# Kernel tuning notes

Measured on AMD Instinct MI355X. Metric: run time of the kernel, lower is better.

## Reference

```python
import jax, jax.numpy as jnp
import numpy as np
from jax import lax

ACTIVE_TOKENS = 256

def setup_inputs() -> dict:
    key = jax.random.key(0)
    k1, k2, k3, k4, k5 = jax.random.split(key, 5)
    B, L, D, A = 8, 4096, 1024, 256
    return {
        "x": jax.random.normal(k1, (B, L, D), dtype=jnp.float32),
        "active": jax.random.normal(k2, (B, A, D), dtype=jnp.float32),
        "cold": jax.random.normal(k3, (B, D), dtype=jnp.float32),
        "w_sal": jax.random.normal(k4, (D,), dtype=jnp.float32) * 0.02,
        "w_read": jax.random.normal(k5, (D, D), dtype=jnp.float32) * 0.02,
    }

def reference(x, active, cold, w_sal, w_read):
    # combined: [B, A+L, D]
    combined = jnp.concatenate([active, x], axis=1)
    B, Lc, D = combined.shape
    keep = min(ACTIVE_TOKENS, Lc)
    # salience head: Linear(D, 1, bias=False) -> [B, Lc]
    salience = jnp.einsum("bld,d->bl", combined, w_sal)
    _, top_idx = lax.top_k(salience, keep)          # [B, keep]
    top_idx = jnp.sort(top_idx, axis=-1)
    # gather kept tokens; torch detaches new_active before use
    kept = jnp.take_along_axis(combined, top_idx[:, :, None], axis=1)  # [B, keep, D]
    new_active = lax.stop_gradient(kept)
    # dropped-token mean (masked_select compaction == total minus kept)
    n_dropped = Lc - keep  # static > 0 here
    dropped_mean = (combined.sum(axis=1) - kept.sum(axis=1)) / n_dropped  # [B, D]
    cold_new = 0.9 * cold + 0.1 * dropped_mean
    # contexts and residual read projection
    active_ctx = new_active.mean(axis=1)            # [B, D]
    ctx = active_ctx + cold_new                      # [B, D]
    x_out = x + jnp.einsum("bd,ed->be", ctx, w_read)[:, None, :]  # Linear: ctx @ W^T
    return x_out, new_active, lax.stop_gradient(cold_new)
```

## Files before the change

kernel.cpp:

```cpp
#include <hip/hip_runtime.h>

#define B 8
#define XROWS 4096
#define AROWS 256
#define LC 4352
#define DD 1024
#define KEEP 256

typedef float vfloat4 __attribute__((ext_vector_type(4)));

__device__ __forceinline__ void nt_store4(const float4& v, float* p) {
    vfloat4 t = {v.x, v.y, v.z, v.w};
    __builtin_nontemporal_store(t, (vfloat4*)p);
}

__device__ __forceinline__ const float* combined_row(const float* __restrict__ x,
                                                     const float* __restrict__ act,
                                                     int b, int l) {
    return (l < AROWS) ? (act + ((size_t)b * AROWS + l) * DD)
                       : (x + ((size_t)b * XROWS + (l - AROWS)) * DD);
}

__global__ __launch_bounds__(256) void k_zero(float* __restrict__ p, int n) {
    int i = blockIdx.x * 256 + threadIdx.x;
    if (i < n) p[i] = 0.0f;
}

__global__ __launch_bounds__(256) void k_sal_sums(
        const float* __restrict__ x, const float* __restrict__ act,
        const float* __restrict__ wsal, float* __restrict__ sal,
        float* __restrict__ sums) {
    const int tid  = threadIdx.x;
    const int wave = tid >> 6;
    const int lane = tid & 63;
    const int b     = blockIdx.x / 136;
    const int chunk = blockIdx.x % 136;
    const int row0  = chunk * 32;
    const int c0 = lane * 4;

    const float4 w0 = *(const float4*)(wsal + 0 * 256 + c0);
    const float4 w1 = *(const float4*)(wsal + 1 * 256 + c0);
    const float4 w2 = *(const float4*)(wsal + 2 * 256 + c0);
    const float4 w3 = *(const float4*)(wsal + 3 * 256 + c0);

    float4 s0 = make_float4(0,0,0,0), s1 = s0, s2 = s0, s3 = s0;

    for (int r = wave; r < 32; r += 4) {
        const int l = row0 + r;
        const float* rp = combined_row(x, act, b, l);
        const float4 a0 = *(const float4*)(rp + 0 * 256 + c0);
        const float4 a1 = *(const float4*)(rp + 1 * 256 + c0);
        const float4 a2 = *(const float4*)(rp + 2 * 256 + c0);
        const float4 a3 = *(const float4*)(rp + 3 * 256 + c0);
        s0.x += a0.x; s0.y += a0.y; s0.z += a0.z; s0.w += a0.w;
        s1.x += a1.x; s1.y += a1.y; s1.z += a1.z; s1.w += a1.w;
        s2.x += a2.x; s2.y += a2.y; s2.z += a2.z; s2.w += a2.w;
        s3.x += a3.x; s3.y += a3.y; s3.z += a3.z; s3.w += a3.w;
        float s = a0.x*w0.x + a0.y*w0.y + a0.z*w0.z + a0.w*w0.w
                + a1.x*w1.x + a1.y*w1.y + a1.z*w1.z + a1.w*w1.w
                + a2.x*w2.x + a2.y*w2.y + a2.z*w2.z + a2.w*w2.w
                + a3.x*w3.x + a3.y*w3.y + a3.z*w3.z + a3.w*w3.w;
        #pragma unroll
        for (int m = 32; m >= 1; m >>= 1) s += __shfl_xor(s, m, 64);
        if (lane == 0) sal[b * LC + l] = s;
    }

    __shared__ float acc[4][DD];
    float* aw = acc[wave];
    *(float4*)(aw + 0 * 256 + c0) = s0;
    *(float4*)(aw + 1 * 256 + c0) = s1;
    *(float4*)(aw + 2 * 256 + c0) = s2;
    *(float4*)(aw + 3 * 256 + c0) = s3;
    __syncthreads();
    const int col = tid * 4;
    float4 t0 = *(const float4*)(acc[0] + col);
    float4 t1 = *(const float4*)(acc[1] + col);
    float4 t2 = *(const float4*)(acc[2] + col);
    float4 t3 = *(const float4*)(acc[3] + col);
    float* sb = sums + b * DD;
    atomicAdd(sb + col + 0, t0.x + t1.x + t2.x + t3.x);
    atomicAdd(sb + col + 1, t0.y + t1.y + t2.y + t3.y);
    atomicAdd(sb + col + 2, t0.z + t1.z + t2.z + t3.z);
    atomicAdd(sb + col + 3, t0.w + t1.w + t2.w + t3.w);
}

__global__ __launch_bounds__(1024) void k_topk(const float* __restrict__ sal,
                                               int* __restrict__ idx,
                                               float* __restrict__ ksum) {
    const int b = blockIdx.x;
    const int tid = threadIdx.x;
    const int lane = tid & 63;
    __shared__ unsigned keys[LC];
    __shared__ int hist[256];
    __shared__ int wtot4[4];
    __shared__ int wtot16[16];
    __shared__ unsigned prefS;
    __shared__ int kremS;

    if (tid < DD) ksum[b * DD + tid] = 0.0f;

    for (int i = tid; i < LC; i += 1024) {
        unsigned u = __float_as_uint(sal[b * LC + i]);
        keys[i] = (u & 0x80000000u) ? ~u : (u | 0x80000000u);
    }
    if (tid == 0) { prefS = 0u; kremS = KEEP; }
    __syncthreads();

    for (int pass = 0; pass < 4; ++pass) {
        const int shift = 24 - 8 * pass;
        if (tid < 256) hist[tid] = 0;
        __syncthreads();
        const unsigned pref = prefS;
        const int krem = kremS;
        for (int i = tid; i < LC; i += 1024) {
            const unsigned k = keys[i];
            if (pass == 0 || (k >> (shift + 8)) == (pref >> (shift + 8)))
                atomicAdd(&hist[(k >> shift) & 255], 1);
        }
        __syncthreads();
        int h = 0, cum = 0;
        if (tid < 256) {
            h = hist[tid];
            cum = h;
            #pragma unroll
            for (int off = 1; off <= 32; off <<= 1) {
                int v = __shfl_down(cum, off, 64);
                if (lane + off < 64) cum += v;
            }
            if (lane == 0) wtot4[tid >> 6] = cum;
        }
        __syncthreads();
        if (tid < 256) {
            for (int w2 = (tid >> 6) + 1; w2 < 4; ++w2) cum += wtot4[w2];
            if (cum >= krem && (cum - h) < krem) {
                prefS = pref | ((unsigned)tid << shift);
                kremS = krem - (cum - h);
            }
        }
        __syncthreads();
    }

    const unsigned T = prefS;
    const int needEQ = kremS;

    const int start = tid * 5;
    const int end = (start + 5 < LC) ? (start + 5) : LC;
    int gt = 0, eq = 0;
    for (int i = start; i < end; ++i) {
        const unsigned k = keys[i];
        gt += (k > T);
        eq += (k == T);
    }
    int packed = (gt << 16) | eq;
    int p = packed;
    #pragma unroll
    for (int off = 1; off <= 32; off <<= 1) {
        int v = __shfl_up(p, off, 64);
        if (lane >= off) p += v;
    }
    if (lane == 63) wtot16[tid >> 6] = p;
    __syncthreads();
    int base = 0;
    for (int w2 = 0; w2 < (tid >> 6); ++w2) base += wtot16[w2];
    const int exc = p - packed + base;
    int gtB = exc >> 16;
    int eqB = exc & 0xFFFF;
    for (int i = start; i < end; ++i) {
        const unsigned k = keys[i];
        if (k > T) {
            idx[b * KEEP + gtB + min(eqB, needEQ)] = i;
            ++gtB;
        } else if (k == T) {
            if (eqB < needEQ) idx[b * KEEP + gtB + eqB] = i;
            ++eqB;
        }
    }
}

__global__ __launch_bounds__(256) void k_gather(const float* __restrict__ x,
        const float* __restrict__ act, const int* __restrict__ idx,
        float* __restrict__ out_active, float* __restrict__ ksum) {
    const int b = blockIdx.x >> 3;
    const int chunk = blockIdx.x & 7;
    const int tid = threadIdx.x;
    const int c4 = tid * 4;
    float4 cs = make_float4(0,0,0,0);
    for (int r = 0; r < 32; ++r) {
        const int k = chunk * 32 + r;
        const int l = idx[b * KEEP + k];
        const float4 v = *(const float4*)(combined_row(x, act, b, l) + c4);
        nt_store4(v, out_active + ((size_t)b * KEEP + k) * DD + c4);
        cs.x += v.x; cs.y += v.y; cs.z += v.z; cs.w += v.w;
    }
    float* kb = ksum + b * DD;
    atomicAdd(kb + c4 + 0, cs.x);
    atomicAdd(kb + c4 + 1, cs.y);
    atomicAdd(kb + c4 + 2, cs.z);
    atomicAdd(kb + c4 + 3, cs.w);
}

__global__ __launch_bounds__(256) void k_read(const float* __restrict__ sums,
        const float* __restrict__ ksum, const float* __restrict__ cold,
        const float* __restrict__ wread, float* __restrict__ rvec,
        float* __restrict__ out_cold) {
    const int e = blockIdx.x;
    const int tid = threadIdx.x;
    const int wave = tid >> 6;
    const int lane = tid & 63;
    const int c4 = tid * 4;
    __shared__ float ctxs[B][DD];
    __shared__ float part[4][B];

    #pragma unroll
    for (int bb = 0; bb < B; ++bb) {
        const float4 s  = *(const float4*)(sums + bb * DD + c4);
        const float4 ks = *(const float4*)(ksum + bb * DD + c4);
        const float4 cd = *(const float4*)(cold + bb * DD + c4);
        float4 cn, cx;
        cn.x = 0.9f * cd.x + 0.1f * ((s.x - ks.x) * (1.0f / 4096.0f));
        cn.y = 0.9f * cd.y + 0.1f * ((s.y - ks.y) * (1.0f / 4096.0f));
        cn.z = 0.9f * cd.z + 0.1f * ((s.z - ks.z) * (1.0f / 4096.0f));
        cn.w = 0.9f * cd.w + 0.1f * ((s.w - ks.w) * (1.0f / 4096.0f));
        cx.x = ks.x * (1.0f / 256.0f) + cn.x;
        cx.y = ks.y * (1.0f / 256.0f) + cn.y;
        cx.z = ks.z * (1.0f / 256.0f) + cn.z;
        cx.w = ks.w * (1.0f / 256.0f) + cn.w;
        *(float4*)(&ctxs[bb][c4]) = cx;
        if (e == 0) *(float4*)(out_cold + bb * DD + c4) = cn;
    }
    __syncthreads();

    const float4 w = *(const float4*)(wread + (size_t)e * DD + c4);
    float p[B];
    #pragma unroll
    for (int bb = 0; bb < B; ++bb) {
        const float4 c = *(const float4*)(&ctxs[bb][c4]);
        p[bb] = w.x*c.x + w.y*c.y + w.z*c.z + w.w*c.w;
    }
    #pragma unroll
    for (int bb = 0; bb < B; ++bb) {
        #pragma unroll
        for (int m = 32; m >= 1; m >>= 1) p[bb] += __shfl_xor(p[bb], m, 64);
        if (lane == 0) part[wave][bb] = p[bb];
    }
    __syncthreads();
    if (tid < B) rvec[tid * DD + e] = part[0][tid] + part[1][tid] + part[2][tid] + part[3][tid];
}

__global__ __launch_bounds__(256) void k_xout(const float* __restrict__ x,
        const float* __restrict__ rvec, float* __restrict__ xout) {
    const size_t total = (size_t)B * XROWS * (DD / 4);
    const float4* x4 = (const float4*)x;
    const float4* r4 = (const float4*)rvec;
    float* of = (float*)xout;
    for (size_t i = (size_t)blockIdx.x * 256 + threadIdx.x; i < total;
         i += (size_t)gridDim.x * 256) {
        float4 v = x4[i];
        const int e4 = (int)(i & 255);
        const int bb = (int)(i >> 20);
        const float4 r = r4[(bb << 8) | e4];
        v.x += r.x; v.y += r.y; v.z += r.z; v.w += r.w;
        nt_store4(v, of + i * 4);
    }
}

extern "C" void kernel_launch(void* const* d_in, const int* in_sizes, int n_in,
                              void* d_out, int out_size, void* d_ws, size_t ws_size,
                              hipStream_t stream) {
    (void)in_sizes; (void)n_in; (void)out_size; (void)ws_size;
    const float* x     = (const float*)d_in[0];
    const float* act   = (const float*)d_in[1];
    const float* cold  = (const float*)d_in[2];
    const float* wsal  = (const float*)d_in[3];
    const float* wread = (const float*)d_in[4];

    float* out        = (float*)d_out;
    float* xout       = out;
    float* out_active = xout + (size_t)B * XROWS * DD;
    float* out_cold   = out_active + (size_t)B * KEEP * DD;

    float* ws   = (float*)d_ws;
    float* sal  = ws;
    float* sums = sal + B * LC;
    float* ksum = sums + B * DD;
    float* rvec = ksum + B * DD;
    int*   idx  = (int*)(rvec + B * DD);

    k_zero<<<(B * DD + 255) / 256, 256, 0, stream>>>(sums, B * DD);
    k_sal_sums<<<B * 136, 256, 0, stream>>>(x, act, wsal, sal, sums);
    k_topk<<<B, 1024, 0, stream>>>(sal, idx, ksum);
    k_gather<<<B * 8, 256, 0, stream>>>(x, act, idx, out_active, ksum);
    k_read<<<DD, 256, 0, stream>>>(sums, ksum, cold, wread, rvec, out_cold);
    k_xout<<<8192, 256, 0, stream>>>(x, rvec, xout);
}
```

Baseline: 305.8 us.

## Fuse all stages into one cooperative persistent kernel with grid syncs

Replaces the six separate launches (zero, salience/sums, top-k, gather, read projection, x_out) with a single cooperative kernel of 256 blocks of 1024 threads, separated by grid.sync barriers. Block-level partial sums are reduced in shared memory before atomics, and zeroing of the accumulators moves into the first phase. The aim is to remove launch gaps and inter-kernel tails. The cost is fewer resident blocks in the bandwidth-heavy phases, only 8 of 256 blocks doing work during top-k, and the overhead of grid-wide barriers.

```diff
diff --git a/kernel.cpp b/kernel.cpp
--- a/kernel.cpp
+++ b/kernel.cpp
@@ -1,4 +1,7 @@
 #include <hip/hip_runtime.h>
+#include <hip/hip_cooperative_groups.h>
+
+namespace cg = cooperative_groups;
 
 #define B 8
 #define XROWS 4096
@@ -6,6 +9,9 @@
 #define LC 4352
 #define DD 1024
 #define KEEP 256
+#define NBLK 256
+#define NTHR 1024
+#define P1ROWS 136
 
 typedef float vfloat4 __attribute__((ext_vector_type(4)));
 
@@ -21,246 +27,263 @@
                        : (x + ((size_t)b * XROWS + (l - AROWS)) * DD);
 }
 
-__global__ __launch_bounds__(256) void k_zero(float* __restrict__ p, int n) {
-    int i = blockIdx.x * 256 + threadIdx.x;
-    if (i < n) p[i] = 0.0f;
-}
-
-__global__ __launch_bounds__(256) void k_sal_sums(
+__global__ __launch_bounds__(NTHR, 4) void k_fused(
         const float* __restrict__ x, const float* __restrict__ act,
-        const float* __restrict__ wsal, float* __restrict__ sal,
-        float* __restrict__ sums) {
+        const float* __restrict__ cold, const float* __restrict__ wsal,
+        const float* __restrict__ wread,
+        float* __restrict__ xout, float* __restrict__ out_active,
+        float* __restrict__ out_cold,
+        float* __restrict__ sal, float* __restrict__ sums,
+        float* __restrict__ ksum, float* __restrict__ rvec,
+        int* __restrict__ idx) {
+    cg::grid_group grid = cg::this_grid();
+    __shared__ __align__(16) char smem[36864];
+
+    const int nb   = blockIdx.x;
     const int tid  = threadIdx.x;
     const int wave = tid >> 6;
     const int lane = tid & 63;
-    const int b     = blockIdx.x / 136;
-    const int chunk = blockIdx.x % 136;
-    const int row0  = chunk * 32;
-    const int c0 = lane * 4;
-
-    const float4 w0 = *(const float4*)(wsal + 0 * 256 + c0);
-    const float4 w1 = *(const float4*)(wsal + 1 * 256 + c0);
-    const float4 w2 = *(const float4*)(wsal + 2 * 256 + c0);
-    const float4 w3 = *(const float4*)(wsal + 3 * 256 + c0);
-
-    float4 s0 = make_float4(0,0,0,0), s1 = s0, s2 = s0, s3 = s0;
-
-    for (int r = wave; r < 32; r += 4) {
-        const int l = row0 + r;
-        const float* rp = combined_row(x, act, b, l);
-        const float4 a0 = *(const float4*)(rp + 0 * 256 + c0);
-        const float4 a1 = *(const float4*)(rp + 1 * 256 + c0);
-        const float4 a2 = *(const float4*)(rp + 2 * 256 + c0);
-        const float4 a3 = *(const float4*)(rp + 3 * 256 + c0);
-        s0.x += a0.x; s0.y += a0.y; s0.z += a0.z; s0.w += a0.w;
-        s1.x += a1.x; s1.y += a1.y; s1.z += a1.z; s1.w += a1.w;
-        s2.x += a2.x; s2.y += a2.y; s2.z += a2.z; s2.w += a2.w;
-        s3.x += a3.x; s3.y += a3.y; s3.z += a3.z; s3.w += a3.w;
-        float s = a0.x*w0.x + a0.y*w0.y + a0.z*w0.z + a0.w*w0.w
-                + a1.x*w1.x + a1.y*w1.y + a1.z*w1.z + a1.w*w1.w
-                + a2.x*w2.x + a2.y*w2.y + a2.z*w2.z + a2.w*w2.w
-                + a3.x*w3.x + a3.y*w3.y + a3.z*w3.z + a3.w*w3.w;
+    const int b     = nb >> 5;
+    const int chunk = nb & 31;
+
+    float fsum;
+    {
+        const int c0 = lane * 4;
+        const float4 w0 = *(const float4*)(wsal + 0 * 256 + c0);
+        const float4 w1 = *(const float4*)(wsal + 1 * 256 + c0);
+        const float4 w2 = *(const float4*)(wsal + 2 * 256 + c0);
+        const float4 w3 = *(const float4*)(wsal + 3 * 256 + c0);
+
+        float4 s0 = make_float4(0,0,0,0), s1 = s0, s2 = s0, s3 = s0;
+        const int row0 = chunk * P1ROWS;
+
+        for (int r = wave; r < P1ROWS; r += 16) {
+            const int l = row0 + r;
+            const float* rp = combined_row(x, act, b, l);
+            const float4 a0 = *(const float4*)(rp + 0 * 256 + c0);
+            const float4 a1 = *(const float4*)(rp + 1 * 256 + c0);
+            const float4 a2 = *(const float4*)(rp + 2 * 256 + c0);
+            const float4 a3 = *(const float4*)(rp + 3 * 256 + c0);
+            s0.x += a0.x; s0.y += a0.y; s0.z += a0.z; s0.w += a0.w;
+            s1.x += a1.x; s1.y += a1.y; s1.z += a1.z; s1.w += a1.w;
+            s2.x += a2.x; s2.y += a2.y; s2.z += a2.z; s2.w += a2.w;
+            s3.x += a3.x; s3.y += a3.y; s3.z += a3.z; s3.w += a3.w;
+            float s = a0.x*w0.x + a0.y*w0.y + a0.z*w0.z + a0.w*w0.w
+                    + a1.x*w1.x + a1.y*w1.y + a1.z*w1.z + a1.w*w1.w
+                    + a2.x*w2.x + a2.y*w2.y + a2.z*w2.z + a2.w*w2.w
+                    + a3.x*w3.x + a3.y*w3.y + a3.z*w3.z + a3.w*w3.w;
+            #pragma unroll
+            for (int m = 32; m >= 1; m >>= 1) s += __shfl_xor(s, m, 64);
+            if (lane == 0) sal[b * LC + l] = s;
+        }
+
+        float* acc = (float*)smem;
+        if (wave < 8) {
+            float* aw = acc + wave * DD;
+            *(float4*)(aw + 0 * 256 + c0) = s0;
+            *(float4*)(aw + 1 * 256 + c0) = s1;
+            *(float4*)(aw + 2 * 256 + c0) = s2;
+            *(float4*)(aw + 3 * 256 + c0) = s3;
+        }
+        __syncthreads();
+        if (wave >= 8) {
+            float* aw = acc + (wave - 8) * DD;
+            float4* p0 = (float4*)(aw + 0 * 256 + c0);
+            float4* p1 = (float4*)(aw + 1 * 256 + c0);
+            float4* p2 = (float4*)(aw + 2 * 256 + c0);
+            float4* p3 = (float4*)(aw + 3 * 256 + c0);
+            float4 t0 = *p0, t1 = *p1, t2 = *p2, t3 = *p3;
+            t0.x += s0.x; t0.y += s0.y; t0.z += s0.z; t0.w += s0.w;
+            t1.x += s1.x; t1.y += s1.y; t1.z += s1.z; t1.w += s1.w;
+            t2.x += s2.x; t2.y += s2.y; t2.z += s2.z; t2.w += s2.w;
+            t3.x += s3.x; t3.y += s3.y; t3.z += s3.z; t3.w += s3.w;
+            *p0 = t0; *p1 = t1; *p2 = t2; *p3 = t3;
+        }
+        __syncthreads();
+        fsum = 0.0f;
         #pragma unroll
-        for (int m = 32; m >= 1; m >>= 1) s += __shfl_xor(s, m, 64);
-        if (lane == 0) sal[b * LC + l] = s;
-    }
-
-    __shared__ float acc[4][DD];
-    float* aw = acc[wave];
-    *(float4*)(aw + 0 * 256 + c0) = s0;
-    *(float4*)(aw + 1 * 256 + c0) = s1;
-    *(float4*)(aw + 2 * 256 + c0) = s2;
-    *(float4*)(aw + 3 * 256 + c0) = s3;
-    __syncthreads();
-    const int col = tid * 4;
-    float4 t0 = *(const float4*)(acc[0] + col);
-    float4 t1 = *(const float4*)(acc[1] + col);
-    float4 t2 = *(const float4*)(acc[2] + col);
-    float4 t3 = *(const float4*)(acc[3] + col);
-    float* sb = sums + b * DD;
-    atomicAdd(sb + col + 0, t0.x + t1.x + t2.x + t3.x);
-    atomicAdd(sb + col + 1, t0.y + t1.y + t2.y + t3.y);
-    atomicAdd(sb + col + 2, t0.z + t1.z + t2.z + t3.z);
-    atomicAdd(sb + col + 3, t0.w + t1.w + t2.w + t3.w);
-}
-
-__global__ __launch_bounds__(1024) void k_topk(const float* __restrict__ sal,
-                                               int* __restrict__ idx,
-                                               float* __restrict__ ksum) {
-    const int b = blockIdx.x;
-    const int tid = threadIdx.x;
-    const int lane = tid & 63;
-    __shared__ unsigned keys[LC];
-    __shared__ int hist[256];
-    __shared__ int wtot4[4];
-    __shared__ int wtot16[16];
-    __shared__ unsigned prefS;
-    __shared__ int kremS;
-
-    if (tid < DD) ksum[b * DD + tid] = 0.0f;
-
-    for (int i = tid; i < LC; i += 1024) {
-        unsigned u = __float_as_uint(sal[b * LC + i]);
-        keys[i] = (u & 0x80000000u) ? ~u : (u | 0x80000000u);
-    }
-    if (tid == 0) { prefS = 0u; kremS = KEEP; }
-    __syncthreads();
-
-    for (int pass = 0; pass < 4; ++pass) {
-        const int shift = 24 - 8 * pass;
-        if (tid < 256) hist[tid] = 0;
-        __syncthreads();
-        const unsigned pref = prefS;
-        const int krem = kremS;
-        for (int i = tid; i < LC; i += 1024) {
+        for (int w = 0; w < 8; ++w) fsum += acc[w * DD + tid];
+
+        if (nb < 8)       sums[nb * DD + tid]       = 0.0f;
+        else if (nb < 16) ksum[(nb - 8) * DD + tid] = 0.0f;
+    }
+    grid.sync();
+
+    atomicAdd(&sums[b * DD + tid], fsum);
+
+    if (nb < 8) {
+        unsigned* keys  = (unsigned*)smem;
+        int*      hist  = (int*)(smem + 17408);
+        int*      wtot4 = (int*)(smem + 18432);
+        int*      wtot16= (int*)(smem + 18448);
+        unsigned* prefS = (unsigned*)(smem + 18512);
+        int*      kremS = (int*)(smem + 18516);
+
+        for (int i = tid; i < LC; i += NTHR) {
+            unsigned u = __float_as_uint(sal[nb * LC + i]);
+            keys[i] = (u & 0x80000000u) ? ~u : (u | 0x80000000u);
+        }
+        if (tid == 0) { *prefS = 0u; *kremS = KEEP; }
+        __syncthreads();
+
+        for (int pass = 0; pass < 4; ++pass) {
+            const int shift = 24 - 8 * pass;
+            if (tid < 256) hist[tid] = 0;
+            __syncthreads();
+            const unsigned pref = *prefS;
+            const int krem = *kremS;
+            for (int i = tid; i < LC; i += NTHR) {
+                const unsigned k = keys[i];
+                if (pass == 0 || (k >> (shift + 8)) == (pref >> (shift + 8)))
+                    atomicAdd(&hist[(k >> shift) & 255], 1);
+            }
+            __syncthreads();
+            int h = 0, cum = 0;
+            if (tid < 256) {
+                h = hist[tid];
+                cum = h;
+                #pragma unroll
+                for (int off = 1; off <= 32; off <<= 1) {
+                    int v = __shfl_down(cum, off, 64);
+                    if (lane + off < 64) cum += v;
+                }
+                if (lane == 0) wtot4[wave] = cum;
+            }
+            __syncthreads();
+            if (tid < 256) {
+                for (int w2 = wave + 1; w2 < 4; ++w2) cum += wtot4[w2];
+                if (cum >= krem && (cum - h) < krem) {
+                    *prefS = pref | ((unsigned)tid << shift);
+                    *kremS = krem - (cum - h);
+                }
+            }
+            __syncthreads();
+        }
+
+        const unsigned T = *prefS;
+        const int needEQ = *kremS;
+
+        const int start = tid * 5;
+        const int end = (start + 5 < LC) ? (start + 5) : LC;
+        int gt = 0, eq = 0;
+        for (int i = start; i < end; ++i) {
             const unsigned k = keys[i];
-            if (pass == 0 || (k >> (shift + 8)) == (pref >> (shift + 8)))
-                atomicAdd(&hist[(k >> shift) & 255], 1);
-        }
-        __syncthreads();
-        int h = 0, cum = 0;
-        if (tid < 256) {
-            h = hist[tid];
-            cum = h;
+            gt += (k > T);
+            eq += (k == T);
+        }
+        int packed = (gt << 16) | eq;
+        int p = packed;
+        #pragma unroll
+        for (int off = 1; off <= 32; off <<= 1) {
+            int v = __shfl_up(p, off, 64);
+            if (lane >= off) p += v;
+        }
+        if (lane == 63) wtot16[wave] = p;
+        __syncthreads();
+        int base = 0;
+        for (int w2 = 0; w2 < wave; ++w2) base += wtot16[w2];
+        const int exc = p - packed + base;
+        int gtB = exc >> 16;
+        int eqB = exc & 0xFFFF;
+        for (int i = start; i < end; ++i) {
+            const unsigned k = keys[i];
+            if (k > T) {
+                idx[nb * KEEP + gtB + min(eqB, needEQ)] = i;
+                ++gtB;
+            } else if (k == T) {
+                if (eqB < needEQ) idx[nb * KEEP + gtB + eqB] = i;
+                ++eqB;
+            }
+        }
+    }
+    grid.sync();
+
+    {
+        const int q  = tid >> 8;
+        const int tq = tid & 255;
+        const int c4 = tq * 4;
+        float4 cs = make_float4(0,0,0,0);
+        #pragma unroll
+        for (int t = 0; t < 2; ++t) {
+            const int rr = q + t * 4;
+            const int k = (chunk << 3) + rr;
+            const int l = idx[b * KEEP + k];
+            const float4 v = *(const float4*)(combined_row(x, act, b, l) + c4);
+            nt_store4(v, out_active + ((size_t)b * KEEP + k) * DD + c4);
+            cs.x += v.x; cs.y += v.y; cs.z += v.z; cs.w += v.w;
+        }
+        float* red = (float*)smem;
+        *(float4*)(red + q * DD + c4) = cs;
+        __syncthreads();
+        if (q == 0) {
+            float4 t0 = *(const float4*)(red + 0 * DD + c4);
+            float4 t1 = *(const float4*)(red + 1 * DD + c4);
+            float4 t2 = *(const float4*)(red + 2 * DD + c4);
+            float4 t3 = *(const float4*)(red + 3 * DD + c4);
+            float* kb = ksum + b * DD;
+            atomicAdd(kb + c4 + 0, t0.x + t1.x + t2.x + t3.x);
+            atomicAdd(kb + c4 + 1, t0.y + t1.y + t2.y + t3.y);
+            atomicAdd(kb + c4 + 2, t0.z + t1.z + t2.z + t3.z);
+            atomicAdd(kb + c4 + 3, t0.w + t1.w + t2.w + t3.w);
+        }
+    }
+    grid.sync();
+
+    {
+        float* ctx  = (float*)smem;
+        float* part = (float*)(smem + 32768);
+        #pragma unroll
+        for (int bb = 0; bb < B; ++bb) {
+            const float s = sums[bb * DD + tid];
+            const float k = ksum[bb * DD + tid];
+            const float c = cold[bb * DD + tid];
+            const float cn = 0.9f * c + 0.1f * ((s - k) * (1.0f / 4096.0f));
+            const float cx = k * (1.0f / 256.0f) + cn;
+            ctx[bb * DD + tid] = cx;
+            if (nb == 0) out_cold[bb * DD + tid] = cn;
+        }
+        __syncthreads();
+        for (int j = 0; j < 4; ++j) {
+            const int e = (nb << 2) | j;
+            const float w = wread[(size_t)e * DD + tid];
+            float pv[B];
             #pragma unroll
-            for (int off = 1; off <= 32; off <<= 1) {
-                int v = __shfl_down(cum, off, 64);
-                if (lane + off < 64) cum += v;
-            }
-            if (lane == 0) wtot4[tid >> 6] = cum;
-        }
-        __syncthreads();
-        if (tid < 256) {
-            for (int w2 = (tid >> 6) + 1; w2 < 4; ++w2) cum += wtot4[w2];
-            if (cum >= krem && (cum - h) < krem) {
-                prefS = pref | ((unsigned)tid << shift);
-                kremS = krem - (cum - h);
-            }
-        }
-        __syncthreads();
-    }
-
-    const unsigned T = prefS;
-    const int needEQ = kremS;
-
-    const int start = tid * 5;
-    const int end = (start + 5 < LC) ? (start + 5) : LC;
-    int gt = 0, eq = 0;
-    for (int i = start; i < end; ++i) {
-        const unsigned k = keys[i];
-        gt += (k > T);
-        eq += (k == T);
-    }
-    int packed = (gt << 16) | eq;
-    int p = packed;
-    #pragma unroll
-    for (int off = 1; off <= 32; off <<= 1) {
-        int v = __shfl_up(p, off, 64);
-        if (lane >= off) p += v;
-    }
-    if (lane == 63) wtot16[tid >> 6] = p;
-    __syncthreads();
-    int base = 0;
-    for (int w2 = 0; w2 < (tid >> 6); ++w2) base += wtot16[w2];
-    const int exc = p - packed + base;
-    int gtB = exc >> 16;
-    int eqB = exc & 0xFFFF;
-    for (int i = start; i < end; ++i) {
-        const unsigned k = keys[i];
-        if (k > T) {
-            idx[b * KEEP + gtB + min(eqB, needEQ)] = i;
-            ++gtB;
-        } else if (k == T) {
-            if (eqB < needEQ) idx[b * KEEP + gtB + eqB] = i;
-            ++eqB;
-        }
-    }
-}
-
-__global__ __launch_bounds__(256) void k_gather(const float* __restrict__ x,
-        const float* __restrict__ act, const int* __restrict__ idx,
-        float* __restrict__ out_active, float* __restrict__ ksum) {
-    const int b = blockIdx.x >> 3;
-    const int chunk = blockIdx.x & 7;
-    const int tid = threadIdx.x;
-    const int c4 = tid * 4;
-    float4 cs = make_float4(0,0,0,0);
-    for (int r = 0; r < 32; ++r) {
-        const int k = chunk * 32 + r;
-        const int l = idx[b * KEEP + k];
-        const float4 v = *(const float4*)(combined_row(x, act, b, l) + c4);
-        nt_store4(v, out_active + ((size_t)b * KEEP + k) * DD + c4);
-        cs.x += v.x; cs.y += v.y; cs.z += v.z; cs.w += v.w;
-    }
-    float* kb = ksum + b * DD;
-    atomicAdd(kb + c4 + 0, cs.x);
-    atomicAdd(kb + c4 + 1, cs.y);
-    atomicAdd(kb + c4 + 2, cs.z);
-    atomicAdd(kb + c4 + 3, cs.w);
-}
-
-__global__ __launch_bounds__(256) void k_read(const float* __restrict__ sums,
-        const float* __restrict__ ksum, const float* __restrict__ cold,
-        const float* __restrict__ wread, float* __restrict__ rvec,
-        float* __restrict__ out_cold) {
-    const int e = blockIdx.x;
-    const int tid = threadIdx.x;
-    const int wave = tid >> 6;
-    const int lane = tid & 63;
-    const int c4 = tid * 4;
-    __shared__ float ctxs[B][DD];
-    __shared__ float part[4][B];
-
-    #pragma unroll
-    for (int bb = 0; bb < B; ++bb) {
-        const float4 s  = *(const float4*)(sums + bb * DD + c4);
-        const float4 ks = *(const float4*)(ksum + bb * DD + c4);
-        const float4 cd = *(const float4*)(cold + bb * DD + c4);
-        float4 cn, cx;
-        cn.x = 0.9f * cd.x + 0.1f * ((s.x - ks.x) * (1.0f / 4096.0f));
-        cn.y = 0.9f * cd.y + 0.1f * ((s.y - ks.y) * (1.0f / 4096.0f));
-        cn.z = 0.9f * cd.z + 0.1f * ((s.z - ks.z) * (1.0f / 4096.0f));
-        cn.w = 0.9f * cd.w + 0.1f * ((s.w - ks.w) * (1.0f / 4096.0f));
-        cx.x = ks.x * (1.0f / 256.0f) + cn.x;
-        cx.y = ks.y * (1.0f / 256.0f) + cn.y;
-        cx.z = ks.z * (1.0f / 256.0f) + cn.z;
-        cx.w = ks.w * (1.0f / 256.0f) + cn.w;
-        *(float4*)(&ctxs[bb][c4]) = cx;
-        if (e == 0) *(float4*)(out_cold + bb * DD + c4) = cn;
-    }
-    __syncthreads();
-
-    const float4 w = *(const float4*)(wread + (size_t)e * DD + c4);
-    float p[B];
-    #pragma unroll
-    for (int bb = 0; bb < B; ++bb) {
-        const float4 c = *(const float4*)(&ctxs[bb][c4]);
-        p[bb] = w.x*c.x + w.y*c.y + w.z*c.z + w.w*c.w;
-    }
-    #pragma unroll
-    for (int bb = 0; bb < B; ++bb) {
-        #pragma unroll
-        for (int m = 32; m >= 1; m >>= 1) p[bb] += __shfl_xor(p[bb], m, 64);
-        if (lane == 0) part[wave][bb] = p[bb];
-    }
-    __syncthreads();
-    if (tid < B) rvec[tid * DD + e] = part[0][tid] + part[1][tid] + part[2][tid] + part[3][tid];
-}
-
-__global__ __launch_bounds__(256) void k_xout(const float* __restrict__ x,
-        const float* __restrict__ rvec, float* __restrict__ xout) {
-    const size_t total = (size_t)B * XROWS * (DD / 4);
-    const float4* x4 = (const float4*)x;
-    const float4* r4 = (const float4*)rvec;
-    float* of = (float*)xout;
-    for (size_t i = (size_t)blockIdx.x * 256 + threadIdx.x; i < total;
-         i += (size_t)gridDim.x * 256) {
-        float4 v = x4[i];
-        const int e4 = (int)(i & 255);
-        const int bb = (int)(i >> 20);
-        const float4 r = r4[(bb << 8) | e4];
-        v.x += r.x; v.y += r.y; v.z += r.z; v.w += r.w;
-        nt_store4(v, of + i * 4);
+            for (int bb = 0; bb < B; ++bb) {
+                float p = w * ctx[bb * DD + tid];
+                #pragma unroll
+                for (int m = 32; m >= 1; m >>= 1) p += __shfl_xor(p, m, 64);
+                pv[bb] = p;
+            }
+            if (lane == 0) {
+                #pragma unroll
+                for (int bb = 0; bb < B; ++bb) part[wave * B + bb] = pv[bb];
+            }
+            __syncthreads();
+            if (tid < B) {
+                float r = 0.0f;
+                #pragma unroll
+                for (int w2 = 0; w2 < 16; ++w2) r += part[w2 * B + tid];
+                rvec[tid * DD + e] = r;
+            }
+            __syncthreads();
+        }
+    }
+    grid.sync();
+
+    {
+        const size_t total = (size_t)B * XROWS * (DD / 4);
+        const float4* x4 = (const float4*)x;
+        const float4* r4 = (const float4*)rvec;
+        float* of = (float*)xout;
+        for (size_t i = (size_t)nb * NTHR + tid; i < total;
+             i += (size_t)NBLK * NTHR) {
+            float4 v = x4[i];
+            const int e4 = (int)(i & 255);
+            const int bb = (int)(i >> 20);
+            const float4 r = r4[(bb << 8) | e4];
+            v.x += r.x; v.y += r.y; v.z += r.z; v.w += r.w;
+            nt_store4(v, of + i * 4);
+        }
     }
 }
 
@@ -286,10 +309,11 @@
     float* rvec = ksum + B * DD;
     int*   idx  = (int*)(rvec + B * DD);
 
-    k_zero<<<(B * DD + 255) / 256, 256, 0, stream>>>(sums, B * DD);
-    k_sal_sums<<<B * 136, 256, 0, stream>>>(x, act, wsal, sal, sums);
-    k_topk<<<B, 1024, 0, stream>>>(sal, idx, ksum);
-    k_gather<<<B * 8, 256, 0, stream>>>(x, act, idx, out_active, ksum);
-    k_read<<<DD, 256, 0, stream>>>(sums, ksum, cold, wread, rvec, out_cold);
-    k_xout<<<8192, 256, 0, stream>>>(x, rvec, xout);
+    void* params[] = {
+        (void*)&x, (void*)&act, (void*)&cold, (void*)&wsal, (void*)&wread,
+        (void*)&xout, (void*)&out_active, (void*)&out_cold,
+        (void*)&sal, (void*)&sums, (void*)&ksum, (void*)&rvec, (void*)&idx
+    };
+    hipLaunchCooperativeKernel((const void*)k_fused, dim3(NBLK), dim3(NTHR),
+                               params, 0, stream);
 }
```

New measurement: 417.8 us. +36.6%, slower.
